# Optimization experiments

Hardware: AMD Instinct MI355X
Metric: run time of the kernel (lower is better)

Reference implementation:

```python
import jax, jax.numpy as jnp
import numpy as np

B, T, C, H = 2, 2048, 768, 12
HD = C // H


def setup_inputs() -> dict:
    key = jax.random.key(0)
    ks = jax.random.split(key, 8)
    s = 0.02
    return {
        "x": jax.random.normal(ks[0], (B, T, C), dtype=jnp.float32),
        "attn_mask1": jax.random.randint(ks[1], (B, T), 0, 2, dtype=jnp.int32),
        "Wq": jax.random.normal(ks[2], (C, C), dtype=jnp.float32) * s,
        "bq": jnp.zeros((C,), dtype=jnp.float32),
        "Wk": jax.random.normal(ks[3], (C, C), dtype=jnp.float32) * s,
        "bk": jnp.zeros((C,), dtype=jnp.float32),
        "Wv": jax.random.normal(ks[4], (C, C), dtype=jnp.float32) * s,
        "bv": jnp.zeros((C,), dtype=jnp.float32),
        "Wp": jax.random.normal(ks[5], (C, C), dtype=jnp.float32) * s,
        "bp": jnp.zeros((C,), dtype=jnp.float32),
    }


def reference(x, attn_mask1, Wq, bq, Wk, bk, Wv, bv, Wp, bp):
    b, t, c = x.shape
    # linear projections, split heads -> [B, H, T, HD]
    def heads(w, bias):
        return (x @ w.T + bias).reshape(b, t, H, HD).transpose(0, 2, 1, 3)
    q = heads(Wq, bq)
    k = heads(Wk, bk)
    v = heads(Wv, bv)
    scale = 1.0 / jnp.sqrt(jnp.asarray(HD, dtype=x.dtype))
    att = jnp.einsum("bhqd,bhkd->bhqk", q, k) * scale  # [B,H,T,T]
    # key-padding mask: original tiles [B,T] along the query axis only
    key_mask = (attn_mask1 == 0)[:, None, None, :]  # [B,1,1,T]
    att = jnp.where(key_mask, -jnp.inf, att)
    att = jax.nn.softmax(att, axis=-1)
    y = jnp.einsum("bhqk,bhkd->bhqd", att, v)  # [B,H,T,HD]
    y = y.transpose(0, 2, 1, 3).reshape(b, t, c)
    return y @ Wp.T + bp
```

## Files before the change

### kernel.cpp

```cpp
#include <hip/hip_runtime.h>
#include <stdint.h>

typedef unsigned short u16;
typedef __bf16 bf16x8 __attribute__((ext_vector_type(8)));
typedef float f32x4 __attribute__((ext_vector_type(4)));

#define BB 2
#define TT 2048
#define CC 768
#define HH 12
#define HD 64
#define MTOT (BB*TT)
#define N_QKV (3*CC)

__device__ __forceinline__ u16 f2bf(float f) {
    uint32_t u = __builtin_bit_cast(uint32_t, f);
    u = (u + 0x7fffu + ((u >> 16) & 1u)) >> 16;
    return (u16)u;
}
__device__ __forceinline__ float bf2f(u16 h) {
    return __builtin_bit_cast(float, (uint32_t)h << 16);
}

union U16x8 { uint4 v; u16 s[8]; };

__device__ __forceinline__ void gl_lds16(const u16* g, u16* l) {
    __builtin_amdgcn_global_load_lds(
        (const __attribute__((address_space(1))) uint32_t*)g,
        (__attribute__((address_space(3))) uint32_t*)l, 16, 0, 0);
}

__global__ void k_cvt(const float* __restrict__ src, u16* __restrict__ dst, int n4) {
    int i = blockIdx.x * blockDim.x + threadIdx.x;
    if (i >= n4) return;
    float4 v = reinterpret_cast<const float4*>(src)[i];
    uint lo = (uint)f2bf(v.x) | ((uint)f2bf(v.y) << 16);
    uint hi = (uint)f2bf(v.z) | ((uint)f2bf(v.w) << 16);
    reinterpret_cast<uint2*>(dst)[i] = make_uint2(lo, hi);
}

__global__ void k_mask(const int* __restrict__ m, float* __restrict__ o, int n) {
    int i = blockIdx.x * blockDim.x + threadIdx.x;
    if (i < n) o[i] = (m[i] == 0) ? -1e30f : 0.0f;
}

__global__ void k_packb(const float* __restrict__ bq, const float* __restrict__ bk,
                        const float* __restrict__ bv, float* __restrict__ o) {
    int i = blockIdx.x * blockDim.x + threadIdx.x;
    if (i < CC) o[i] = bq[i];
    else if (i < 2 * CC) o[i] = bk[i - CC];
    else if (i < 3 * CC) o[i] = bv[i - 2 * CC];
}

#define GBM 128
#define GBN 128
#define GBK 32

__global__ __launch_bounds__(256)
void k_gemm(const u16* __restrict__ A, const u16* __restrict__ W,
            const float* __restrict__ bias, int K, int N, int mode,
            u16* __restrict__ outQ, u16* __restrict__ outK, u16* __restrict__ outVt,
            float* __restrict__ outLin)
{
    __shared__ alignas(16) u16 As[GBM][GBK];
    __shared__ alignas(16) u16 Bs[GBN][GBK];

    const int tid  = threadIdx.x;
    const int lane = tid & 63;
    const int wave = tid >> 6;
    const int m0 = blockIdx.y * GBM;
    const int n0 = blockIdx.x * GBN;
    const int wm = (wave >> 1) * 64;
    const int wn = (wave & 1) * 64;

    f32x4 acc[4][4];
#pragma unroll
    for (int m = 0; m < 4; ++m)
#pragma unroll
        for (int n = 0; n < 4; ++n)
            acc[m][n] = f32x4{0.f, 0.f, 0.f, 0.f};

    const int lrow = lane >> 2;
    const int lcol = (lane & 3) * 8;

    for (int k0 = 0; k0 < K; k0 += GBK) {
        __syncthreads();
        {
            const int r0 = wave * 32;
            gl_lds16(A + (size_t)(m0 + r0 + lrow) * K + k0 + lcol,      &As[r0][0]);
            gl_lds16(A + (size_t)(m0 + r0 + 16 + lrow) * K + k0 + lcol, &As[r0 + 16][0]);
            gl_lds16(W + (size_t)(n0 + r0 + lrow) * K + k0 + lcol,      &Bs[r0][0]);
            gl_lds16(W + (size_t)(n0 + r0 + 16 + lrow) * K + k0 + lcol, &Bs[r0 + 16][0]);
        }
        __syncthreads();

        bf16x8 af[4], bfb[4];
#pragma unroll
        for (int m = 0; m < 4; ++m)
            af[m] = *reinterpret_cast<const bf16x8*>(&As[wm + m * 16 + (lane & 15)][(lane >> 4) * 8]);
#pragma unroll
        for (int n = 0; n < 4; ++n)
            bfb[n] = *reinterpret_cast<const bf16x8*>(&Bs[wn + n * 16 + (lane & 15)][(lane >> 4) * 8]);
#pragma unroll
        for (int m = 0; m < 4; ++m)
#pragma unroll
            for (int n = 0; n < 4; ++n)
                acc[m][n] = __builtin_amdgcn_mfma_f32_16x16x32_bf16(af[m], bfb[n], acc[m][n], 0, 0, 0);
    }

    const int col   = lane & 15;
    const int rbase = (lane >> 4) * 4;
#pragma unroll
    for (int m = 0; m < 4; ++m) {
#pragma unroll
        for (int n = 0; n < 4; ++n) {
            const int gn = n0 + wn + n * 16 + col;
            const float bv = bias[gn];
#pragma unroll
            for (int j = 0; j < 4; ++j) {
                const int gm = m0 + wm + m * 16 + rbase + j;
                const float val = acc[m][n][j] + bv;
                if (mode == 1) {
                    outLin[(size_t)gm * N + gn] = val;
                } else {
                    const int proj = gn / CC;
                    const int c = gn - proj * CC;
                    const int h = c >> 6, hd = c & 63;
                    const int b = gm >> 11, t = gm & (TT - 1);
                    if (proj == 0)
                        outQ[((size_t)(b * HH + h) * TT + t) * HD + hd] = f2bf(val);
                    else if (proj == 1)
                        outK[((size_t)(b * HH + h) * TT + t) * HD + hd] = f2bf(val);
                    else
                        outVt[((size_t)(b * HH + h) * HD + hd) * TT + t] = f2bf(val);
                }
            }
        }
    }
}

__global__ __launch_bounds__(64)
void k_attn(const u16* __restrict__ Qh, const u16* __restrict__ Kh,
            const u16* __restrict__ Vt, const float* __restrict__ maskb,
            u16* __restrict__ Y)
{
    __shared__ alignas(16) u16 Ps[32][136];

    const int lane = threadIdx.x;
    const int raw  = blockIdx.x;
    const int virt = (raw & 7) * 192 + (raw >> 3);
    const int bh = virt >> 6;
    const int b  = bh / HH, h = bh % HH;
    const int q0 = (virt & 63) * 32;

    const u16* Qp = Qh + (size_t)bh * TT * HD;
    const u16* Kp = Kh + (size_t)bh * TT * HD;
    const u16* Vp = Vt + (size_t)bh * HD * TT;
    const float* mrow = maskb + b * TT;

    const int l15 = lane & 15;
    const int lg  = lane >> 4;

    bf16x8 qf[2][2];
#pragma unroll
    for (int m = 0; m < 2; ++m)
#pragma unroll
        for (int ks = 0; ks < 2; ++ks) {
            U16x8 t;
            t.v = *reinterpret_cast<const uint4*>(
                Qp + (size_t)(q0 + m * 16 + l15) * HD + ks * 32 + lg * 8);
            U16x8 o;
#pragma unroll
            for (int j = 0; j < 8; ++j) o.s[j] = f2bf(bf2f(t.s[j]) * 0.125f);
            qf[m][ks] = __builtin_bit_cast(bf16x8, o.v);
        }

    f32x4 oacc[2][4];
#pragma unroll
    for (int m = 0; m < 2; ++m)
#pragma unroll
        for (int n = 0; n < 4; ++n) oacc[m][n] = f32x4{0.f, 0.f, 0.f, 0.f};
    float mrun[2][4], lrun[2][4];
#pragma unroll
    for (int m = 0; m < 2; ++m)
#pragma unroll
        for (int j = 0; j < 4; ++j) { mrun[m][j] = -1e30f; lrun[m][j] = 0.f; }

    for (int kt = 0; kt < TT; kt += 128) {
        f32x4 sacc[2][8];
#pragma unroll
        for (int m = 0; m < 2; ++m)
#pragma unroll
            for (int n = 0; n < 8; ++n) sacc[m][n] = f32x4{0.f, 0.f, 0.f, 0.f};
#pragma unroll
        for (int ks = 0; ks < 2; ++ks) {
            uint4 kfr[8];
#pragma unroll
            for (int n = 0; n < 8; ++n)
                kfr[n] = *reinterpret_cast<const uint4*>(
                    Kp + (size_t)(kt + n * 16 + l15) * HD + ks * 32 + lg * 8);
#pragma unroll
            for (int n = 0; n < 8; ++n) {
                bf16x8 kf = __builtin_bit_cast(bf16x8, kfr[n]);
#pragma unroll
                for (int m = 0; m < 2; ++m)
                    sacc[m][n] = __builtin_amdgcn_mfma_f32_16x16x32_bf16(qf[m][ks], kf, sacc[m][n], 0, 0, 0);
            }
        }

        float mbv[8];
#pragma unroll
        for (int n = 0; n < 8; ++n) mbv[n] = mrow[kt + n * 16 + l15];

        float tmax[2][4];
#pragma unroll
        for (int m = 0; m < 2; ++m)
#pragma unroll
            for (int j = 0; j < 4; ++j) tmax[m][j] = -1e30f;
#pragma unroll
        for (int m = 0; m < 2; ++m)
#pragma unroll
            for (int n = 0; n < 8; ++n)
#pragma unroll
                for (int j = 0; j < 4; ++j) {
                    float s = sacc[m][n][j] + mbv[n];
                    sacc[m][n][j] = s;
                    tmax[m][j] = fmaxf(tmax[m][j], s);
                }
#pragma unroll
        for (int off = 1; off < 16; off <<= 1)
#pragma unroll
            for (int m = 0; m < 2; ++m)
#pragma unroll
                for (int j = 0; j < 4; ++j)
                    tmax[m][j] = fmaxf(tmax[m][j], __shfl_xor(tmax[m][j], off));

        float scl[2][4];
#pragma unroll
        for (int m = 0; m < 2; ++m)
#pragma unroll
            for (int j = 0; j < 4; ++j) {
                float mnew = fmaxf(mrun[m][j], tmax[m][j]);
                scl[m][j] = __expf(mrun[m][j] - mnew);
                mrun[m][j] = mnew;
            }

        float rs[2][4];
#pragma unroll
        for (int m = 0; m < 2; ++m)
#pragma unroll
            for (int j = 0; j < 4; ++j) rs[m][j] = 0.f;
#pragma unroll
        for (int m = 0; m < 2; ++m)
#pragma unroll
            for (int n = 0; n < 8; ++n)
#pragma unroll
                for (int j = 0; j < 4; ++j) {
                    float s = sacc[m][n][j];
                    float p = (s < -1e29f) ? 0.f : __expf(s - mrun[m][j]);
                    sacc[m][n][j] = p;
                    rs[m][j] += p;
                }
#pragma unroll
        for (int off = 1; off < 16; off <<= 1)
#pragma unroll
            for (int m = 0; m < 2; ++m)
#pragma unroll
                for (int j = 0; j < 4; ++j) rs[m][j] += __shfl_xor(rs[m][j], off);
#pragma unroll
        for (int m = 0; m < 2; ++m)
#pragma unroll
            for (int j = 0; j < 4; ++j) lrun[m][j] = lrun[m][j] * scl[m][j] + rs[m][j];

#pragma unroll
        for (int m = 0; m < 2; ++m)
#pragma unroll
            for (int n = 0; n < 8; ++n)
#pragma unroll
                for (int j = 0; j < 4; ++j)
                    Ps[m * 16 + lg * 4 + j][n * 16 + l15] = f2bf(sacc[m][n][j]);

#pragma unroll
        for (int m = 0; m < 2; ++m)
#pragma unroll
            for (int n = 0; n < 4; ++n)
#pragma unroll
                for (int j = 0; j < 4; ++j) oacc[m][n][j] *= scl[m][j];

#pragma unroll
        for (int ks2 = 0; ks2 < 4; ++ks2) {
            bf16x8 pf[2];
#pragma unroll
            for (int m = 0; m < 2; ++m)
                pf[m] = *reinterpret_cast<const bf16x8*>(&Ps[m * 16 + l15][ks2 * 32 + lg * 8]);
            uint4 vfr[4];
#pragma unroll
            for (int n = 0; n < 4; ++n)
                vfr[n] = *reinterpret_cast<const uint4*>(
                    Vp + (size_t)(n * 16 + l15) * TT + kt + ks2 * 32 + lg * 8);
#pragma unroll
            for (int n = 0; n < 4; ++n) {
                bf16x8 vf = __builtin_bit_cast(bf16x8, vfr[n]);
#pragma unroll
                for (int m = 0; m < 2; ++m)
                    oacc[m][n] = __builtin_amdgcn_mfma_f32_16x16x32_bf16(pf[m], vf, oacc[m][n], 0, 0, 0);
            }
        }
    }

#pragma unroll
    for (int m = 0; m < 2; ++m)
#pragma unroll
        for (int n = 0; n < 4; ++n)
#pragma unroll
            for (int j = 0; j < 4; ++j) {
                const int t = q0 + m * 16 + lg * 4 + j;
                const int c = h * 64 + n * 16 + l15;
                Y[((size_t)b * TT + t) * CC + c] = f2bf(oacc[m][n][j] / lrun[m][j]);
            }
}

extern "C" void kernel_launch(void* const* d_in, const int* in_sizes, int n_in,
                              void* d_out, int out_size, void* d_ws, size_t ws_size,
                              hipStream_t stream)
{
    const float* x    = (const float*)d_in[0];
    const int*   mask = (const int*)d_in[1];
    const float* Wq   = (const float*)d_in[2];
    const float* bq   = (const float*)d_in[3];
    const float* Wk   = (const float*)d_in[4];
    const float* bk   = (const float*)d_in[5];
    const float* Wv   = (const float*)d_in[6];
    const float* bv   = (const float*)d_in[7];
    const float* Wp   = (const float*)d_in[8];
    const float* bp   = (const float*)d_in[9];
    float* out = (float*)d_out;

    char* w = (char*)d_ws;
    auto alloc = [&](size_t bytes) {
        char* p = w;
        w += (bytes + 255) & ~(size_t)255;
        return p;
    };
    u16* x_bf    = (u16*)alloc((size_t)MTOT * CC * 2);
    u16* wqkv_bf = (u16*)alloc((size_t)3 * CC * CC * 2);
    u16* wp_bf   = (u16*)alloc((size_t)CC * CC * 2);
    u16* qh      = (u16*)alloc((size_t)MTOT * CC * 2);
    u16* kh      = (u16*)alloc((size_t)MTOT * CC * 2);
    u16* vt      = (u16*)alloc((size_t)MTOT * CC * 2);
    u16* y_bf    = (u16*)alloc((size_t)MTOT * CC * 2);
    float* maskb = (float*)alloc((size_t)BB * TT * 4);
    float* bqkv  = (float*)alloc((size_t)N_QKV * 4);

    const int NX4 = MTOT * CC / 4;
    k_cvt<<<(NX4 + 255) / 256, 256, 0, stream>>>(x, x_bf, NX4);
    const int NW4 = CC * CC / 4;
    k_cvt<<<(NW4 + 255) / 256, 256, 0, stream>>>(Wq, wqkv_bf, NW4);
    k_cvt<<<(NW4 + 255) / 256, 256, 0, stream>>>(Wk, wqkv_bf + (size_t)CC * CC, NW4);
    k_cvt<<<(NW4 + 255) / 256, 256, 0, stream>>>(Wv, wqkv_bf + (size_t)2 * CC * CC, NW4);
    k_cvt<<<(NW4 + 255) / 256, 256, 0, stream>>>(Wp, wp_bf, NW4);
    k_mask<<<(BB * TT + 255) / 256, 256, 0, stream>>>(mask, maskb, BB * TT);
    k_packb<<<(N_QKV + 255) / 256, 256, 0, stream>>>(bq, bk, bv, bqkv);

    k_gemm<<<dim3(N_QKV / GBN, MTOT / GBM), 256, 0, stream>>>(
        x_bf, wqkv_bf, bqkv, CC, N_QKV, 0, qh, kh, vt, nullptr);

    k_attn<<<dim3(1536), 64, 0, stream>>>(qh, kh, vt, maskb, y_bf);

    k_gemm<<<dim3(CC / GBN, MTOT / GBM), 256, 0, stream>>>(
        y_bf, wp_bf, bp, CC, CC, 1, nullptr, nullptr, nullptr, out);
}
```

Baseline: 268.4 us.

## Rewrite attention with 32x32 MFMA in registers and double-buffer GEMM LDS

The attention kernel switches from 16x16 MFMA tiles to 32x32x16 MFMA with a transposed formulation (S^T = K·Q^T). Softmax reductions now run mostly inside registers, and P passes to the PV MFMA through lane shuffles with packed bf16 converts instead of an LDS round trip. The key tile shrinks from 128 to 32 per iteration. Separately, the GEMM double-buffers its LDS tiles, issuing the next tile's loads before computing on the current one, and drops one barrier per iteration. Risks include more loop iterations with less work each, and the removal of the explicit masked-to-zero guard, which now depends on the exp of a very negative number underflowing to zero.

```diff
diff --git a/kernel.cpp b/kernel.cpp
--- a/kernel.cpp
+++ b/kernel.cpp
@@ -4,6 +4,7 @@
 typedef unsigned short u16;
 typedef __bf16 bf16x8 __attribute__((ext_vector_type(8)));
 typedef float f32x4 __attribute__((ext_vector_type(4)));
+typedef float f32x16 __attribute__((ext_vector_type(16)));
 
 #define BB 2
 #define TT 2048
@@ -62,8 +63,8 @@
             u16* __restrict__ outQ, u16* __restrict__ outK, u16* __restrict__ outVt,
             float* __restrict__ outLin)
 {
-    __shared__ alignas(16) u16 As[GBM][GBK];
-    __shared__ alignas(16) u16 Bs[GBN][GBK];
+    __shared__ alignas(16) u16 As[2][GBM][GBK];
+    __shared__ alignas(16) u16 Bs[2][GBM][GBK];
 
     const int tid  = threadIdx.x;
     const int lane = tid & 63;
@@ -83,29 +84,37 @@
     const int lrow = lane >> 2;
     const int lcol = (lane & 3) * 8;
 
-    for (int k0 = 0; k0 < K; k0 += GBK) {
-        __syncthreads();
-        {
-            const int r0 = wave * 32;
-            gl_lds16(A + (size_t)(m0 + r0 + lrow) * K + k0 + lcol,      &As[r0][0]);
-            gl_lds16(A + (size_t)(m0 + r0 + 16 + lrow) * K + k0 + lcol, &As[r0 + 16][0]);
-            gl_lds16(W + (size_t)(n0 + r0 + lrow) * K + k0 + lcol,      &Bs[r0][0]);
-            gl_lds16(W + (size_t)(n0 + r0 + 16 + lrow) * K + k0 + lcol, &Bs[r0 + 16][0]);
-        }
-        __syncthreads();
+    auto stage = [&](int buf, int k0) {
+        const int r0 = wave * 32;
+        gl_lds16(A + (size_t)(m0 + r0 + lrow) * K + k0 + lcol,      &As[buf][r0][0]);
+        gl_lds16(A + (size_t)(m0 + r0 + 16 + lrow) * K + k0 + lcol, &As[buf][r0 + 16][0]);
+        gl_lds16(W + (size_t)(n0 + r0 + lrow) * K + k0 + lcol,      &Bs[buf][r0][0]);
+        gl_lds16(W + (size_t)(n0 + r0 + 16 + lrow) * K + k0 + lcol, &Bs[buf][r0 + 16][0]);
+    };
+
+    const int nt = K / GBK;
+    stage(0, 0);
+    __syncthreads();
+
+    int cur = 0;
+    for (int t = 0; t < nt; ++t) {
+        if (t + 1 < nt) stage(cur ^ 1, (t + 1) * GBK);
 
         bf16x8 af[4], bfb[4];
 #pragma unroll
         for (int m = 0; m < 4; ++m)
-            af[m] = *reinterpret_cast<const bf16x8*>(&As[wm + m * 16 + (lane & 15)][(lane >> 4) * 8]);
+            af[m] = *reinterpret_cast<const bf16x8*>(&As[cur][wm + m * 16 + (lane & 15)][(lane >> 4) * 8]);
 #pragma unroll
         for (int n = 0; n < 4; ++n)
-            bfb[n] = *reinterpret_cast<const bf16x8*>(&Bs[wn + n * 16 + (lane & 15)][(lane >> 4) * 8]);
+            bfb[n] = *reinterpret_cast<const bf16x8*>(&Bs[cur][wn + n * 16 + (lane & 15)][(lane >> 4) * 8]);
 #pragma unroll
         for (int m = 0; m < 4; ++m)
 #pragma unroll
             for (int n = 0; n < 4; ++n)
                 acc[m][n] = __builtin_amdgcn_mfma_f32_16x16x32_bf16(af[m], bfb[n], acc[m][n], 0, 0, 0);
+
+        __syncthreads();
+        cur ^= 1;
     }
 
     const int col   = lane & 15;
@@ -144,8 +153,6 @@
             const u16* __restrict__ Vt, const float* __restrict__ maskb,
             u16* __restrict__ Y)
 {
-    __shared__ alignas(16) u16 Ps[32][136];
-
     const int lane = threadIdx.x;
     const int raw  = blockIdx.x;
     const int virt = (raw & 7) * 192 + (raw >> 3);
@@ -153,171 +160,127 @@
     const int b  = bh / HH, h = bh % HH;
     const int q0 = (virt & 63) * 32;
 
+    const int l31 = lane & 31;
+    const int hi  = lane >> 5;
+
     const u16* Qp = Qh + (size_t)bh * TT * HD;
     const u16* Kp = Kh + (size_t)bh * TT * HD;
     const u16* Vp = Vt + (size_t)bh * HD * TT;
     const float* mrow = maskb + b * TT;
 
-    const int l15 = lane & 15;
-    const int lg  = lane >> 4;
-
-    bf16x8 qf[2][2];
-#pragma unroll
-    for (int m = 0; m < 2; ++m)
-#pragma unroll
-        for (int ks = 0; ks < 2; ++ks) {
-            U16x8 t;
-            t.v = *reinterpret_cast<const uint4*>(
-                Qp + (size_t)(q0 + m * 16 + l15) * HD + ks * 32 + lg * 8);
-            U16x8 o;
-#pragma unroll
-            for (int j = 0; j < 8; ++j) o.s[j] = f2bf(bf2f(t.s[j]) * 0.125f);
-            qf[m][ks] = __builtin_bit_cast(bf16x8, o.v);
-        }
-
-    f32x4 oacc[2][4];
-#pragma unroll
-    for (int m = 0; m < 2; ++m)
-#pragma unroll
-        for (int n = 0; n < 4; ++n) oacc[m][n] = f32x4{0.f, 0.f, 0.f, 0.f};
-    float mrun[2][4], lrun[2][4];
-#pragma unroll
-    for (int m = 0; m < 2; ++m)
-#pragma unroll
-        for (int j = 0; j < 4; ++j) { mrun[m][j] = -1e30f; lrun[m][j] = 0.f; }
-
-    for (int kt = 0; kt < TT; kt += 128) {
-        f32x4 sacc[2][8];
-#pragma unroll
-        for (int m = 0; m < 2; ++m)
-#pragma unroll
-            for (int n = 0; n < 8; ++n) sacc[m][n] = f32x4{0.f, 0.f, 0.f, 0.f};
-#pragma unroll
-        for (int ks = 0; ks < 2; ++ks) {
-            uint4 kfr[8];
-#pragma unroll
-            for (int n = 0; n < 8; ++n)
-                kfr[n] = *reinterpret_cast<const uint4*>(
-                    Kp + (size_t)(kt + n * 16 + l15) * HD + ks * 32 + lg * 8);
-#pragma unroll
-            for (int n = 0; n < 8; ++n) {
-                bf16x8 kf = __builtin_bit_cast(bf16x8, kfr[n]);
-#pragma unroll
-                for (int m = 0; m < 2; ++m)
-                    sacc[m][n] = __builtin_amdgcn_mfma_f32_16x16x32_bf16(qf[m][ks], kf, sacc[m][n], 0, 0, 0);
-            }
-        }
-
-        float mbv[8];
-#pragma unroll
-        for (int n = 0; n < 8; ++n) mbv[n] = mrow[kt + n * 16 + l15];
-
-        float tmax[2][4];
-#pragma unroll
-        for (int m = 0; m < 2; ++m)
-#pragma unroll
-            for (int j = 0; j < 4; ++j) tmax[m][j] = -1e30f;
-#pragma unroll
-        for (int m = 0; m < 2; ++m)
-#pragma unroll
-            for (int n = 0; n < 8; ++n)
-#pragma unroll
-                for (int j = 0; j < 4; ++j) {
-                    float s = sacc[m][n][j] + mbv[n];
-                    sacc[m][n][j] = s;
-                    tmax[m][j] = fmaxf(tmax[m][j], s);
-                }
-#pragma unroll
-        for (int off = 1; off < 16; off <<= 1)
-#pragma unroll
-            for (int m = 0; m < 2; ++m)
-#pragma unroll
-                for (int j = 0; j < 4; ++j)
-                    tmax[m][j] = fmaxf(tmax[m][j], __shfl_xor(tmax[m][j], off));
-
-        float scl[2][4];
-#pragma unroll
-        for (int m = 0; m < 2; ++m)
-#pragma unroll
-            for (int j = 0; j < 4; ++j) {
-                float mnew = fmaxf(mrun[m][j], tmax[m][j]);
-                scl[m][j] = __expf(mrun[m][j] - mnew);
-                mrun[m][j] = mnew;
-            }
-
-        float rs[2][4];
-#pragma unroll
-        for (int m = 0; m < 2; ++m)
-#pragma unroll
-            for (int j = 0; j < 4; ++j) rs[m][j] = 0.f;
-#pragma unroll
-        for (int m = 0; m < 2; ++m)
-#pragma unroll
-            for (int n = 0; n < 8; ++n)
-#pragma unroll
-                for (int j = 0; j < 4; ++j) {
-                    float s = sacc[m][n][j];
-                    float p = (s < -1e29f) ? 0.f : __expf(s - mrun[m][j]);
-                    sacc[m][n][j] = p;
-                    rs[m][j] += p;
-                }
-#pragma unroll
-        for (int off = 1; off < 16; off <<= 1)
-#pragma unroll
-            for (int m = 0; m < 2; ++m)
-#pragma unroll
-                for (int j = 0; j < 4; ++j) rs[m][j] += __shfl_xor(rs[m][j], off);
-#pragma unroll
-        for (int m = 0; m < 2; ++m)
-#pragma unroll
-            for (int j = 0; j < 4; ++j) lrun[m][j] = lrun[m][j] * scl[m][j] + rs[m][j];
-
-#pragma unroll
-        for (int m = 0; m < 2; ++m)
-#pragma unroll
-            for (int n = 0; n < 8; ++n)
-#pragma unroll
-                for (int j = 0; j < 4; ++j)
-                    Ps[m * 16 + lg * 4 + j][n * 16 + l15] = f2bf(sacc[m][n][j]);
-
-#pragma unroll
-        for (int m = 0; m < 2; ++m)
-#pragma unroll
-            for (int n = 0; n < 4; ++n)
-#pragma unroll
-                for (int j = 0; j < 4; ++j) oacc[m][n][j] *= scl[m][j];
-
-#pragma unroll
-        for (int ks2 = 0; ks2 < 4; ++ks2) {
-            bf16x8 pf[2];
-#pragma unroll
-            for (int m = 0; m < 2; ++m)
-                pf[m] = *reinterpret_cast<const bf16x8*>(&Ps[m * 16 + l15][ks2 * 32 + lg * 8]);
-            uint4 vfr[4];
-#pragma unroll
-            for (int n = 0; n < 4; ++n)
-                vfr[n] = *reinterpret_cast<const uint4*>(
-                    Vp + (size_t)(n * 16 + l15) * TT + kt + ks2 * 32 + lg * 8);
-#pragma unroll
-            for (int n = 0; n < 4; ++n) {
-                bf16x8 vf = __builtin_bit_cast(bf16x8, vfr[n]);
-#pragma unroll
-                for (int m = 0; m < 2; ++m)
-                    oacc[m][n] = __builtin_amdgcn_mfma_f32_16x16x32_bf16(pf[m], vf, oacc[m][n], 0, 0, 0);
-            }
-        }
-    }
-
-#pragma unroll
-    for (int m = 0; m < 2; ++m)
-#pragma unroll
-        for (int n = 0; n < 4; ++n)
-#pragma unroll
-            for (int j = 0; j < 4; ++j) {
-                const int t = q0 + m * 16 + lg * 4 + j;
-                const int c = h * 64 + n * 16 + l15;
-                Y[((size_t)b * TT + t) * CC + c] = f2bf(oacc[m][n][j] / lrun[m][j]);
-            }
+    bf16x8 qf[4];
+#pragma unroll
+    for (int i = 0; i < 4; ++i) {
+        U16x8 t;
+        t.v = *reinterpret_cast<const uint4*>(Qp + (size_t)(q0 + l31) * HD + 16 * i + hi * 8);
+        U16x8 o;
+#pragma unroll
+        for (int j = 0; j < 8; ++j) o.s[j] = f2bf(bf2f(t.s[j]) * 0.125f);
+        qf[i] = __builtin_bit_cast(bf16x8, o.v);
+    }
+
+    f32x16 oacc0, oacc1;
+#pragma unroll
+    for (int r = 0; r < 16; ++r) { oacc0[r] = 0.f; oacc1[r] = 0.f; }
+    float mrun = -1e30f, lrun = 0.f;
+
+    for (int kt = 0; kt < TT; kt += 32) {
+        f32x16 s;
+#pragma unroll
+        for (int r = 0; r < 16; ++r) s[r] = 0.f;
+#pragma unroll
+        for (int i = 0; i < 4; ++i) {
+            uint4 kv = *reinterpret_cast<const uint4*>(
+                Kp + (size_t)(kt + l31) * HD + 16 * i + hi * 8);
+            s = __builtin_amdgcn_mfma_f32_32x32x16_bf16(
+                __builtin_bit_cast(bf16x8, kv), qf[i], s, 0, 0, 0);
+        }
+
+        float mbf[16];
+#pragma unroll
+        for (int r2 = 0; r2 < 4; ++r2) {
+            float4 v = *reinterpret_cast<const float4*>(mrow + kt + 8 * r2 + 4 * hi);
+            mbf[4 * r2 + 0] = v.x; mbf[4 * r2 + 1] = v.y;
+            mbf[4 * r2 + 2] = v.z; mbf[4 * r2 + 3] = v.w;
+        }
+#pragma unroll
+        for (int r = 0; r < 16; ++r) s[r] += mbf[r];
+
+        float m8[8];
+#pragma unroll
+        for (int r = 0; r < 8; ++r) m8[r] = fmaxf(s[r], s[r + 8]);
+        float m4[4];
+#pragma unroll
+        for (int r = 0; r < 4; ++r) m4[r] = fmaxf(m8[r], m8[r + 4]);
+        float tm = fmaxf(fmaxf(m4[0], m4[1]), fmaxf(m4[2], m4[3]));
+        tm = fmaxf(tm, __shfl_xor(tm, 32));
+
+        float mnew = fmaxf(mrun, tm);
+        float scl = __expf(mrun - mnew);
+        mrun = mnew;
+
+        float p[16];
+#pragma unroll
+        for (int r = 0; r < 16; ++r) p[r] = __expf(s[r] - mrun);
+        float s8[8];
+#pragma unroll
+        for (int r = 0; r < 8; ++r) s8[r] = p[r] + p[r + 8];
+        float s4[4];
+#pragma unroll
+        for (int r = 0; r < 4; ++r) s4[r] = s8[r] + s8[r + 4];
+        float rs = (s4[0] + s4[1]) + (s4[2] + s4[3]);
+        rs += __shfl_xor(rs, 32);
+        lrun = lrun * scl + rs;
+
+#pragma unroll
+        for (int r = 0; r < 16; ++r) { oacc0[r] *= scl; oacc1[r] *= scl; }
+
+        uint32_t pk[8];
+#pragma unroll
+        for (int g = 0; g < 4; ++g) {
+            asm("v_cvt_pk_bf16_f32 %0, %1, %2"
+                : "=v"(pk[2 * g]) : "v"(p[4 * g]), "v"(p[4 * g + 1]));
+            asm("v_cvt_pk_bf16_f32 %0, %1, %2"
+                : "=v"(pk[2 * g + 1]) : "v"(p[4 * g + 2]), "v"(p[4 * g + 3]));
+        }
+
+#pragma unroll
+        for (int kk = 0; kk < 2; ++kk) {
+            uint32_t sA = (uint32_t)__shfl_xor((int)(hi ? pk[4 * kk]     : pk[4 * kk + 2]), 32);
+            uint32_t sB = (uint32_t)__shfl_xor((int)(hi ? pk[4 * kk + 1] : pk[4 * kk + 3]), 32);
+            uint4 bw;
+            bw.x = hi ? sA : pk[4 * kk];
+            bw.y = hi ? sB : pk[4 * kk + 1];
+            bw.z = hi ? pk[4 * kk + 2] : sA;
+            bw.w = hi ? pk[4 * kk + 3] : sB;
+            bf16x8 pb = __builtin_bit_cast(bf16x8, bw);
+
+            uint4 v0 = *reinterpret_cast<const uint4*>(
+                Vp + (size_t)l31 * TT + kt + 16 * kk + hi * 8);
+            uint4 v1 = *reinterpret_cast<const uint4*>(
+                Vp + (size_t)(32 + l31) * TT + kt + 16 * kk + hi * 8);
+            oacc0 = __builtin_amdgcn_mfma_f32_32x32x16_bf16(
+                __builtin_bit_cast(bf16x8, v0), pb, oacc0, 0, 0, 0);
+            oacc1 = __builtin_amdgcn_mfma_f32_32x32x16_bf16(
+                __builtin_bit_cast(bf16x8, v1), pb, oacc1, 0, 0, 0);
+        }
+    }
+
+    const float inv = 1.0f / lrun;
+    u16* yrow = Y + ((size_t)b * TT + q0 + l31) * CC + h * 64;
+#pragma unroll
+    for (int dt = 0; dt < 2; ++dt) {
+        f32x16 oa = dt ? oacc1 : oacc0;
+#pragma unroll
+        for (int r2 = 0; r2 < 4; ++r2) {
+            ushort4 w;
+            w.x = f2bf(oa[4 * r2 + 0] * inv);
+            w.y = f2bf(oa[4 * r2 + 1] * inv);
+            w.z = f2bf(oa[4 * r2 + 2] * inv);
+            w.w = f2bf(oa[4 * r2 + 3] * inv);
+            *reinterpret_cast<ushort4*>(yrow + dt * 32 + 8 * r2 + 4 * hi) = w;
+        }
+    }
 }
 
 extern "C" void kernel_launch(void* const* d_in, const int* in_sizes, int n_in,
```

Measured after the change: 257.6 us. 1.04x faster.
